# Optimization experiments

Hardware: AMD Instinct MI355X
Metric: run time of the kernel (lower is better)

The kernel has to match this reference:

```python
import jax, jax.numpy as jnp
import numpy as np

N, E, F, H, C, G = 50000, 600000, 128, 128, 10, 500
NUM_GIN = 3
BN_EPS = 1e-5


def _bn(x, gamma, beta):
    # BatchNorm1d in training mode: batch statistics over node/graph dim
    m = jnp.mean(x, axis=0)
    v = jnp.mean((x - m) ** 2, axis=0)
    return (x - m) * jax.lax.rsqrt(v + BN_EPS) * gamma + beta


def setup_inputs() -> dict:
    key = jax.random.key(0)
    ks = jax.random.split(key, 16)
    s = 1.0 / np.sqrt(H)
    inp = {
        "x": jax.random.normal(ks[0], (N, F), dtype=jnp.float32),
        "edge_index": jax.random.randint(ks[1], (2, E), 0, N),
        "batch": jnp.sort(jax.random.randint(ks[2], (N,), 0, G)),
        # bn_feat
        "gamma_feat": jnp.ones((F,), jnp.float32),
        "beta_feat": jnp.full((F,), 1e-4, jnp.float32),
        # conv_feat (GCNConv gfn=True -> pure linear)
        "W_feat": jax.random.uniform(ks[3], (F, H), jnp.float32, -s, s),
        "b_feat": jnp.zeros((H,), jnp.float32),
        # GIN conv MLPs, stacked over 3 layers
        "gin_W1": jax.random.uniform(ks[4], (NUM_GIN, H, H), jnp.float32, -s, s),
        "gin_b1": jnp.zeros((NUM_GIN, H), jnp.float32),
        "gin_gamma": jnp.ones((NUM_GIN, H), jnp.float32),
        "gin_beta": jnp.full((NUM_GIN, H), 1e-4, jnp.float32),
        "gin_W2": jax.random.uniform(ks[5], (NUM_GIN, H, H), jnp.float32, -s, s),
        "gin_b2": jnp.zeros((NUM_GIN, H), jnp.float32),
        # one FC block (num_fc_layers=2 -> 1 bn+lin)
        "gamma_fc": jnp.ones((H,), jnp.float32),
        "beta_fc": jnp.full((H,), 1e-4, jnp.float32),
        "W_fc": jax.random.uniform(ks[6], (H, H), jnp.float32, -s, s),
        "b_fc": jnp.zeros((H,), jnp.float32),
        # bn_hidden + classifier
        "gamma_h": jnp.ones((H,), jnp.float32),
        "beta_h": jnp.full((H,), 1e-4, jnp.float32),
        "W_cls": jax.random.uniform(ks[7], (H, C), jnp.float32, -s, s),
        "b_cls": jnp.zeros((C,), jnp.float32),
    }
    return inp


def reference(x, gamma_feat, beta_feat, W_feat, b_feat,
              gin_W1, gin_b1, gin_gamma, gin_beta, gin_W2, gin_b2,
              gamma_fc, beta_fc, W_fc, b_fc,
              gamma_h, beta_h, W_cls, b_cls,
              edge_index, batch):
    src, dst = edge_index[0], edge_index[1]
    h = _bn(x, gamma_feat, beta_feat)
    h = jax.nn.relu(h @ W_feat + b_feat)  # GCNConv gfn=True == Linear
    for i in range(NUM_GIN):
        # GIN aggregation: (1+eps)*x + sum_{j->i} x_j, eps=0
        agg = jnp.zeros_like(h).at[dst].add(h[src])
        z = h + agg
        z = jax.nn.relu(_bn(z @ gin_W1[i] + gin_b1[i], gin_gamma[i], gin_beta[i]))
        h = jax.nn.relu(z @ gin_W2[i] + gin_b2[i])
    g = jax.ops.segment_sum(h, batch, num_segments=G)  # global_add_pool -> [G,H]
    g = jax.nn.relu(_bn(g, gamma_fc, beta_fc) @ W_fc + b_fc)
    g = _bn(g, gamma_h, beta_h)
    logits = g @ W_cls + b_cls
    return jax.nn.log_softmax(logits, axis=-1)
```

## Files before the change

### kernel.cpp

```cpp
#include <hip/hip_runtime.h>
#include <math.h>

#define N_NODES 50000
#define N_EDGES 600000
#define HDIM 128
#define NCLS 10
#define NGRAPH 500
#define BN_EPS 1e-5f
#define SCAN_BLOCKS 196

typedef short bf16x8 __attribute__((ext_vector_type(8)));
typedef float f32x4 __attribute__((ext_vector_type(4)));

__global__ void colstats_kernel(const float* __restrict__ X, int M, float* __restrict__ stats) {
    int col = threadIdx.x & 127;
    int sub = threadIdx.x >> 7;
    float s = 0.f, sq = 0.f;
    for (int r = blockIdx.x * 2 + sub; r < M; r += gridDim.x * 2) {
        float v = X[(size_t)r * HDIM + col];
        s += v; sq += v * v;
    }
    atomicAdd(&stats[col], s);
    atomicAdd(&stats[HDIM + col], sq);
}

__global__ void hist_kernel(const int* __restrict__ ei, int* __restrict__ counts) {
    int e = blockIdx.x * 256 + threadIdx.x;
    if (e < N_EDGES) atomicAdd(&counts[ei[N_EDGES + e]], 1);
}

__global__ __launch_bounds__(256) void scan1_kernel(const int* __restrict__ counts,
                                                    int* __restrict__ partial,
                                                    int* __restrict__ blockSums) {
    __shared__ int tmp[256];
    int tid = threadIdx.x;
    int i = blockIdx.x * 256 + tid;
    int v = (i < N_NODES) ? counts[i] : 0;
    tmp[tid] = v;
    __syncthreads();
#pragma unroll
    for (int off = 1; off < 256; off <<= 1) {
        int t = (tid >= off) ? tmp[tid - off] : 0;
        __syncthreads();
        tmp[tid] += t;
        __syncthreads();
    }
    if (i < N_NODES) partial[i] = tmp[tid] - v;
    if (tid == 255) blockSums[blockIdx.x] = tmp[255];
}

__global__ __launch_bounds__(256) void scan2_kernel(const int* __restrict__ blockSums,
                                                    int* __restrict__ blockBase) {
    __shared__ int tmp[256];
    int tid = threadIdx.x;
    int v = (tid < SCAN_BLOCKS) ? blockSums[tid] : 0;
    tmp[tid] = v;
    __syncthreads();
#pragma unroll
    for (int off = 1; off < 256; off <<= 1) {
        int t = (tid >= off) ? tmp[tid - off] : 0;
        __syncthreads();
        tmp[tid] += t;
        __syncthreads();
    }
    if (tid < SCAN_BLOCKS) blockBase[tid] = tmp[tid] - v;
}

__global__ __launch_bounds__(256) void scan3_kernel(const int* __restrict__ partial,
                                                    const int* __restrict__ blockBase,
                                                    int* __restrict__ offsets,
                                                    int* __restrict__ cursor) {
    int i = blockIdx.x * 256 + threadIdx.x;
    if (i < N_NODES) {
        int o = partial[i] + blockBase[blockIdx.x];
        offsets[i] = o;
        cursor[i] = o;
    }
    if (i == 0) offsets[N_NODES] = N_EDGES;
}

__global__ void fill_kernel(const int* __restrict__ ei, int* __restrict__ cursor, int* __restrict__ csr) {
    int e = blockIdx.x * 256 + threadIdx.x;
    if (e < N_EDGES) {
        int d = ei[N_EDGES + e];
        int pos = atomicAdd(&cursor[d], 1);
        csr[pos] = ei[e];
    }
}

__global__ __launch_bounds__(256) void agg_kernel(const float* __restrict__ h,
                                                  const int* __restrict__ offsets,
                                                  const int* __restrict__ csr,
                                                  float* __restrict__ z) {
    int node = (blockIdx.x * 256 + threadIdx.x) >> 6;
    int lane = threadIdx.x & 63;
    if (node >= N_NODES) return;
    int c0 = lane * 2;
    int beg = offsets[node], end = offsets[node + 1];
    const float2 self = *(const float2*)&h[(size_t)node * HDIM + c0];
    float ax = self.x, ay = self.y;
    for (int j = beg; j < end; j += 64) {
        int cnt = min(64, end - j);
        int sl = (j + lane < end) ? csr[j + lane] : 0;
        int t = 0;
        for (; t + 4 <= cnt; t += 4) {
            int s0 = __shfl(sl, t, 64);
            int s1 = __shfl(sl, t + 1, 64);
            int s2 = __shfl(sl, t + 2, 64);
            int s3 = __shfl(sl, t + 3, 64);
            float2 v0 = *(const float2*)&h[(size_t)s0 * HDIM + c0];
            float2 v1 = *(const float2*)&h[(size_t)s1 * HDIM + c0];
            float2 v2 = *(const float2*)&h[(size_t)s2 * HDIM + c0];
            float2 v3 = *(const float2*)&h[(size_t)s3 * HDIM + c0];
            ax += v0.x + v1.x + v2.x + v3.x;
            ay += v0.y + v1.y + v2.y + v3.y;
        }
        for (; t < cnt; t++) {
            int s = __shfl(sl, t, 64);
            float2 hv = *(const float2*)&h[(size_t)s * HDIM + c0];
            ax += hv.x; ay += hv.y;
        }
    }
    float2 o; o.x = ax; o.y = ay;
    *(float2*)&z[(size_t)node * HDIM + c0] = o;
}

__global__ __launch_bounds__(128) void segsum2_kernel(const float* __restrict__ h,
                                                      const int* __restrict__ batch,
                                                      float* __restrict__ g) {
    int b = blockIdx.x;
    int tid = threadIdx.x;
    __shared__ int bounds[2];
    if (tid < 2) {
        int target = b + tid;
        int lo = 0, hi = N_NODES;
        while (lo < hi) {
            int mid = (lo + hi) >> 1;
            if (batch[mid] < target) lo = mid + 1; else hi = mid;
        }
        bounds[tid] = lo;
    }
    __syncthreads();
    int beg = bounds[0], end = bounds[1];
    float s = 0.f;
    for (int r = beg; r < end; r++) s += h[(size_t)r * HDIM + tid];
    g[b * HDIM + tid] = s;
}

__device__ inline void dekker_split(float v, unsigned short& hi, unsigned short& lo) {
    unsigned u = __float_as_uint(v);
    hi = (unsigned short)(u >> 16);
    float flo = v - __uint_as_float(u & 0xffff0000u);
    lo = (unsigned short)(__float_as_uint(flo) >> 16);
}

__global__ __launch_bounds__(256) void prep_w(const float* __restrict__ W1,
                                              const float* __restrict__ W2,
                                              unsigned short* __restrict__ wh,
                                              unsigned short* __restrict__ wl) {
    int m = blockIdx.x;
    const float* src = (m < 3) ? (W1 + m * HDIM * HDIM) : (W2 + (m - 3) * HDIM * HDIM);
    unsigned short* dh = wh + m * HDIM * HDIM;
    unsigned short* dl = wl + m * HDIM * HDIM;
    for (int i = threadIdx.x; i < HDIM * HDIM; i += 256) {
        int n = i >> 7, k = i & 127;
        float v = src[k * HDIM + n];
        unsigned short h16, l16;
        dekker_split(v, h16, l16);
        dh[i] = h16; dl[i] = l16;
    }
}

__global__ __launch_bounds__(256) void prep_feat(const float* __restrict__ W,
                                                 const float* __restrict__ bfeat,
                                                 const float* __restrict__ stats,
                                                 const float* __restrict__ gamma,
                                                 const float* __restrict__ beta,
                                                 float invCnt,
                                                 unsigned short* __restrict__ dh,
                                                 unsigned short* __restrict__ dl,
                                                 float* __restrict__ biasF) {
    __shared__ float aP[HDIM], bP[HDIM];
    int tid = threadIdx.x;
    if (tid < HDIM) {
        float m = stats[tid] * invCnt;
        float v = stats[HDIM + tid] * invCnt - m * m;
        float a = gamma[tid] * rsqrtf(v + BN_EPS);
        aP[tid] = a;
        bP[tid] = beta[tid] - m * a;
    }
    __syncthreads();
    for (int i = tid; i < HDIM * HDIM; i += 256) {
        int n = i >> 7, k = i & 127;
        float v = aP[k] * W[k * HDIM + n];
        unsigned short h16, l16;
        dekker_split(v, h16, l16);
        dh[i] = h16; dl[i] = l16;
    }
    if (tid < HDIM) {
        float acc = bfeat[tid];
        for (int k = 0; k < HDIM; k++) acc = fmaf(bP[k], W[k * HDIM + tid], acc);
        biasF[tid] = acc;
    }
}

template <int MODE>
__global__ __launch_bounds__(256, 2) void mfma_gemm(const float* __restrict__ A,
                                                    const unsigned short* __restrict__ Bh,
                                                    const unsigned short* __restrict__ Bl,
                                                    const float* __restrict__ bias,
                                                    float* __restrict__ C, int M,
                                                    const float* __restrict__ statsPre,
                                                    const float* __restrict__ gammaPre,
                                                    const float* __restrict__ betaPre,
                                                    float invCnt,
                                                    float* __restrict__ statsOut) {
    const int tid = threadIdx.x;
    const int w = tid >> 6, l = tid & 63;
    const int q = l >> 4, c16 = l & 15;
    const int rb = blockIdx.x * 128 + w * 32;

    int rowA[2];
#pragma unroll
    for (int rt = 0; rt < 2; rt++) rowA[rt] = min(rb + rt * 16 + c16, M - 1);

    float bs[8];
#pragma unroll
    for (int c = 0; c < 8; c++) bs[c] = bias[c * 16 + c16];

    f32x4 acc[2][8];
#pragma unroll
    for (int rt = 0; rt < 2; rt++)
#pragma unroll
        for (int c = 0; c < 8; c++) acc[rt][c] = (f32x4){0.f, 0.f, 0.f, 0.f};

#pragma unroll
    for (int s = 0; s < 4; s++) {
        const int k0 = s * 32 + q * 8;
        float aK[8], bK[8];
        if (MODE == 2) {
#pragma unroll
            for (int j = 0; j < 8; j++) {
                int k = k0 + j;
                float m = statsPre[k] * invCnt;
                float var = statsPre[HDIM + k] * invCnt - m * m;
                float a = gammaPre[k] * rsqrtf(var + BN_EPS);
                aK[j] = a;
                bK[j] = betaPre[k] - m * a;
            }
        }
        bf16x8 ah[2], al[2];
#pragma unroll
        for (int rt = 0; rt < 2; rt++) {
            const float* ap = A + (size_t)rowA[rt] * HDIM + k0;
            float4 v0 = *(const float4*)ap;
            float4 v1 = *(const float4*)(ap + 4);
            float vv[8] = {v0.x, v0.y, v0.z, v0.w, v1.x, v1.y, v1.z, v1.w};
#pragma unroll
            for (int j = 0; j < 8; j++) {
                float v = vv[j];
                if (MODE == 2) v = fmaxf(fmaf(v, aK[j], bK[j]), 0.f);
                unsigned u = __float_as_uint(v);
                ah[rt][j] = (short)(u >> 16);
                float flo = v - __uint_as_float(u & 0xffff0000u);
                al[rt][j] = (short)(__float_as_uint(flo) >> 16);
            }
        }
#pragma unroll
        for (int c = 0; c < 8; c++) {
            const size_t bo = (size_t)(c * 16 + c16) * HDIM + k0;
            bf16x8 bh = *(const bf16x8*)(Bh + bo);
            bf16x8 bl = *(const bf16x8*)(Bl + bo);
#pragma unroll
            for (int rt = 0; rt < 2; rt++) {
                acc[rt][c] = __builtin_amdgcn_mfma_f32_16x16x32_bf16(ah[rt], bh, acc[rt][c], 0, 0, 0);
                acc[rt][c] = __builtin_amdgcn_mfma_f32_16x16x32_bf16(al[rt], bh, acc[rt][c], 0, 0, 0);
                acc[rt][c] = __builtin_amdgcn_mfma_f32_16x16x32_bf16(ah[rt], bl, acc[rt][c], 0, 0, 0);
            }
        }
    }

    float ssum[8], ssq[8];
    if (MODE == 1) {
#pragma unroll
        for (int c = 0; c < 8; c++) { ssum[c] = 0.f; ssq[c] = 0.f; }
    }
#pragma unroll
    for (int rt = 0; rt < 2; rt++) {
#pragma unroll
        for (int reg = 0; reg < 4; reg++) {
            int row = rb + rt * 16 + q * 4 + reg;
            if (row < M) {
                float* cp = C + (size_t)row * HDIM + c16;
#pragma unroll
                for (int c = 0; c < 8; c++) {
                    float v = acc[rt][c][reg] + bs[c];
                    if (MODE != 1) v = fmaxf(v, 0.f);
                    cp[c * 16] = v;
                    if (MODE == 1) { ssum[c] += v; ssq[c] += v * v; }
                }
            }
        }
    }
    if (MODE == 1) {
#pragma unroll
        for (int c = 0; c < 8; c++) {
            float s2 = ssum[c] + __shfl_xor(ssum[c], 16, 64);
            float s4 = s2 + __shfl_xor(s2, 32, 64);
            float t2 = ssq[c] + __shfl_xor(ssq[c], 16, 64);
            float t4 = t2 + __shfl_xor(t2, 32, 64);
            if (q == 0) {
                atomicAdd(&statsOut[c * 16 + c16], s4);
                atomicAdd(&statsOut[HDIM + c * 16 + c16], t4);
            }
        }
    }
}

template <bool PRE_A, bool PRE_B, bool RELU, bool STATS>
__global__ __launch_bounds__(256, 3) void gemm_bn(const float* A, const float* __restrict__ B,
                                                  const float* __restrict__ bias, float* C, int M,
                                                  const float* __restrict__ statsPre,
                                                  const float* __restrict__ gammaPre,
                                                  const float* __restrict__ betaPre,
                                                  float invCnt, float* __restrict__ statsOut) {
    __shared__ float At[64][65];
    __shared__ float Bs[64][128];
    __shared__ float aPre[128], bPre[128];

    const int tid = threadIdx.x;
    const int tx = tid & 15, ty = tid >> 4;
    const int r0 = blockIdx.x * 64;

    if (PRE_A || PRE_B) {
        if (tid < 128) {
            float m = statsPre[tid] * invCnt;
            float v = statsPre[128 + tid] * invCnt - m * m;
            float a = gammaPre[tid] * rsqrtf(v + BN_EPS);
            aPre[tid] = a;
            bPre[tid] = betaPre[tid] - m * a;
        }
        __syncthreads();
    }

    float acc[4][8];
#pragma unroll
    for (int i = 0; i < 4; i++)
#pragma unroll
        for (int j = 0; j < 8; j++) acc[i][j] = 0.f;

    float biasEff[8];
#pragma unroll
    for (int j = 0; j < 8; j++) biasEff[j] = bias[8 * tx + j];
    if (PRE_B) {
        for (int k = 0; k < 128; k++) {
            float bb = bPre[k];
            const float* Brow = B + (size_t)k * HDIM + 8 * tx;
#pragma unroll
            for (int j = 0; j < 8; j++) biasEff[j] = fmaf(bb, Brow[j], biasEff[j]);
        }
    }

    for (int kc = 0; kc < 128; kc += 64) {
#pragma unroll
        for (int i = 0; i < 4; i++) {
            int f4 = tid + i * 256;
            int row = f4 >> 4;
            int kg = f4 & 15;
            int grow = r0 + row;
            float4 av;
            if (grow < M) av = *(const float4*)(A + (size_t)grow * HDIM + kc + kg * 4);
            else av = make_float4(0.f, 0.f, 0.f, 0.f);
            if (PRE_A) {
                int kb = kc + kg * 4;
                av.x = fmaxf(fmaf(av.x, aPre[kb + 0], bPre[kb + 0]), 0.f);
                av.y = fmaxf(fmaf(av.y, aPre[kb + 1], bPre[kb + 1]), 0.f);
                av.z = fmaxf(fmaf(av.z, aPre[kb + 2], bPre[kb + 2]), 0.f);
                av.w = fmaxf(fmaf(av.w, aPre[kb + 3], bPre[kb + 3]), 0.f);
            }
            At[kg * 4 + 0][row] = av.x;
            At[kg * 4 + 1][row] = av.y;
            At[kg * 4 + 2][row] = av.z;
            At[kg * 4 + 3][row] = av.w;
        }
#pragma unroll
        for (int i = 0; i < 8; i++) {
            int f4 = tid + i * 256;
            int krow = f4 >> 5;
            int cg = f4 & 31;
            float4 bv = *(const float4*)(B + (size_t)(kc + krow) * HDIM + cg * 4);
            if (PRE_B) {
                float s = aPre[kc + krow];
                bv.x *= s; bv.y *= s; bv.z *= s; bv.w *= s;
            }
            *(float4*)&Bs[krow][cg * 4] = bv;
        }
        __syncthreads();
#pragma unroll 8
        for (int k = 0; k < 64; k++) {
            float av[4];
            av[0] = At[k][ty];
            av[1] = At[k][ty + 16];
            av[2] = At[k][ty + 32];
            av[3] = At[k][ty + 48];
            const float4 b0 = *(const float4*)&Bs[k][8 * tx];
            const float4 b1 = *(const float4*)&Bs[k][8 * tx + 4];
            float bv[8] = {b0.x, b0.y, b0.z, b0.w, b1.x, b1.y, b1.z, b1.w};
#pragma unroll
            for (int i = 0; i < 4; i++)
#pragma unroll
                for (int j = 0; j < 8; j++) acc[i][j] = fmaf(av[i], bv[j], acc[i][j]);
        }
        __syncthreads();
    }

    float s[8], sq[8];
    if (STATS) {
#pragma unroll
        for (int j = 0; j < 8; j++) { s[j] = 0.f; sq[j] = 0.f; }
    }
#pragma unroll
    for (int i = 0; i < 4; i++) {
        int grow = r0 + ty + 16 * i;
        if (grow < M) {
            float v[8];
#pragma unroll
            for (int j = 0; j < 8; j++) {
                v[j] = acc[i][j] + biasEff[j];
                if (RELU) v[j] = fmaxf(v[j], 0.f);
                if (STATS) { s[j] += v[j]; sq[j] += v[j] * v[j]; }
            }
            float4 o0 = make_float4(v[0], v[1], v[2], v[3]);
            float4 o1 = make_float4(v[4], v[5], v[6], v[7]);
            *(float4*)(C + (size_t)grow * HDIM + 8 * tx) = o0;
            *(float4*)(C + (size_t)grow * HDIM + 8 * tx + 4) = o1;
        }
    }
    if (STATS) {
        float* red = &At[0][0];
#pragma unroll
        for (int j = 0; j < 8; j++) {
            red[ty * 128 + 8 * tx + j] = s[j];
            red[2048 + ty * 128 + 8 * tx + j] = sq[j];
        }
        __syncthreads();
        if (tid < 128) {
            float t = 0.f;
#pragma unroll
            for (int u = 0; u < 16; u++) t += red[u * 128 + tid];
            atomicAdd(&statsOut[tid], t);
        } else {
            int col = tid - 128;
            float t = 0.f;
#pragma unroll
            for (int u = 0; u < 16; u++) t += red[2048 + u * 128 + col];
            atomicAdd(&statsOut[128 + col], t);
        }
    }
}

__global__ __launch_bounds__(256) void head_kernel(const float* __restrict__ g2,
                                                   const float* __restrict__ stats,
                                                   const float* __restrict__ gamma,
                                                   const float* __restrict__ beta,
                                                   const float* __restrict__ Wc,
                                                   const float* __restrict__ bc,
                                                   float* __restrict__ out, float invCnt) {
    __shared__ float Wf[HDIM * NCLS];
    __shared__ float bf[NCLS];
    __shared__ float aP[HDIM], bP[HDIM];
    const int tid = threadIdx.x;
    if (tid < HDIM) {
        float m = stats[tid] * invCnt;
        float v = stats[HDIM + tid] * invCnt - m * m;
        float a = gamma[tid] * rsqrtf(v + BN_EPS);
        aP[tid] = a;
        bP[tid] = beta[tid] - m * a;
    }
    __syncthreads();
    for (int idx = tid; idx < HDIM * NCLS; idx += 256) {
        int k = idx / NCLS;
        Wf[idx] = aP[k] * Wc[idx];
    }
    if (tid < NCLS) {
        float sv = bc[tid];
        for (int k = 0; k < HDIM; k++) sv = fmaf(bP[k], Wc[k * NCLS + tid], sv);
        bf[tid] = sv;
    }
    __syncthreads();
    int row = blockIdx.x * 256 + tid;
    if (row >= NGRAPH) return;
    float l[NCLS];
#pragma unroll
    for (int c = 0; c < NCLS; c++) l[c] = bf[c];
    for (int k = 0; k < HDIM; k++) {
        float gv = g2[row * HDIM + k];
#pragma unroll
        for (int c = 0; c < NCLS; c++) l[c] = fmaf(gv, Wf[k * NCLS + c], l[c]);
    }
    float mx = l[0];
#pragma unroll
    for (int c = 1; c < NCLS; c++) mx = fmaxf(mx, l[c]);
    float se = 0.f;
#pragma unroll
    for (int c = 0; c < NCLS; c++) se += expf(l[c] - mx);
    float lse = mx + logf(se);
#pragma unroll
    for (int c = 0; c < NCLS; c++) out[row * NCLS + c] = l[c] - lse;
}

extern "C" void kernel_launch(void* const* d_in, const int* in_sizes, int n_in,
                              void* d_out, int out_size, void* d_ws, size_t ws_size,
                              hipStream_t stream) {
    const float* x          = (const float*)d_in[0];
    const int*   ei         = (const int*)d_in[1];
    const int*   batch      = (const int*)d_in[2];
    const float* gamma_feat = (const float*)d_in[3];
    const float* beta_feat  = (const float*)d_in[4];
    const float* W_feat     = (const float*)d_in[5];
    const float* b_feat     = (const float*)d_in[6];
    const float* gin_W1     = (const float*)d_in[7];
    const float* gin_b1     = (const float*)d_in[8];
    const float* gin_gamma  = (const float*)d_in[9];
    const float* gin_beta   = (const float*)d_in[10];
    const float* gin_W2     = (const float*)d_in[11];
    const float* gin_b2     = (const float*)d_in[12];
    const float* gamma_fc   = (const float*)d_in[13];
    const float* beta_fc    = (const float*)d_in[14];
    const float* W_fc       = (const float*)d_in[15];
    const float* b_fc       = (const float*)d_in[16];
    const float* gamma_h    = (const float*)d_in[17];
    const float* beta_h     = (const float*)d_in[18];
    const float* W_cls      = (const float*)d_in[19];
    const float* b_cls      = (const float*)d_in[20];
    float* out = (float*)d_out;

    float* ws = (float*)d_ws;
    size_t off = 0;
    float* h  = ws + off; off += (size_t)N_NODES * HDIM;
    float* zy = ws + off; off += (size_t)N_NODES * HDIM;
    float* g2 = ws + off; off += NGRAPH * HDIM;
    float* g  = ws + off; off += NGRAPH * HDIM;
    size_t zstart = off;
    float* stats = ws + off; off += 256 * 6;
    int* counts = (int*)(ws + off); off += N_NODES;
    size_t zbytes = (off - zstart) * sizeof(float);
    int* offsets   = (int*)(ws + off); off += N_NODES + 1;
    int* cursor    = (int*)(ws + off); off += N_NODES;
    int* csr       = (int*)(ws + off); off += N_EDGES;
    int* partial   = (int*)(ws + off); off += N_NODES;
    int* blockSums = (int*)(ws + off); off += 256;
    int* blockBase = (int*)(ws + off); off += 256;
    off = (off + 3) & ~(size_t)3;
    unsigned short* wt_hi = (unsigned short*)(ws + off); off += 7 * HDIM * HDIM / 2;
    unsigned short* wt_lo = (unsigned short*)(ws + off); off += 7 * HDIM * HDIM / 2;
    float* biasF = ws + off; off += HDIM;

    float* statsX  = stats;
    float* statsYa[3] = {stats + 256, stats + 512, stats + 768};
    float* statsG  = stats + 1024;
    float* statsG2 = stats + 1280;

    hipMemsetAsync(stats, 0, zbytes, stream);

    const float invN = 1.f / (float)N_NODES;
    const float invG = 1.f / (float)NGRAPH;
    const int eblocks = (N_EDGES + 255) / 256;
    const int nwaves  = (N_NODES * 64 + 255) / 256;
    const int mblocks = (N_NODES + 127) / 128;

    prep_w<<<6, 256, 0, stream>>>(gin_W1, gin_W2, wt_hi, wt_lo);
    colstats_kernel<<<256, 256, 0, stream>>>(x, N_NODES, statsX);
    hist_kernel<<<eblocks, 256, 0, stream>>>(ei, counts);
    scan1_kernel<<<SCAN_BLOCKS, 256, 0, stream>>>(counts, partial, blockSums);
    scan2_kernel<<<1, 256, 0, stream>>>(blockSums, blockBase);
    scan3_kernel<<<SCAN_BLOCKS, 256, 0, stream>>>(partial, blockBase, offsets, cursor);
    fill_kernel<<<eblocks, 256, 0, stream>>>(ei, cursor, csr);
    prep_feat<<<1, 256, 0, stream>>>(W_feat, b_feat, statsX, gamma_feat, beta_feat, invN,
                                     wt_hi + 6 * HDIM * HDIM, wt_lo + 6 * HDIM * HDIM, biasF);

    mfma_gemm<0><<<mblocks, 256, 0, stream>>>(
        x, wt_hi + 6 * HDIM * HDIM, wt_lo + 6 * HDIM * HDIM, biasF, h, N_NODES,
        nullptr, nullptr, nullptr, invN, nullptr);

    for (int i = 0; i < 3; i++) {
        agg_kernel<<<nwaves, 256, 0, stream>>>(h, offsets, csr, zy);
        mfma_gemm<1><<<mblocks, 256, 0, stream>>>(
            zy, wt_hi + i * HDIM * HDIM, wt_lo + i * HDIM * HDIM, gin_b1 + i * HDIM,
            zy, N_NODES, nullptr, nullptr, nullptr, invN, statsYa[i]);
        mfma_gemm<2><<<mblocks, 256, 0, stream>>>(
            zy, wt_hi + (3 + i) * HDIM * HDIM, wt_lo + (3 + i) * HDIM * HDIM, gin_b2 + i * HDIM,
            h, N_NODES, statsYa[i], gin_gamma + i * HDIM, gin_beta + i * HDIM, invN, nullptr);
    }

    segsum2_kernel<<<NGRAPH, 128, 0, stream>>>(h, batch, g);
    colstats_kernel<<<8, 256, 0, stream>>>(g, NGRAPH, statsG);
    gemm_bn<false, true, true, true><<<(NGRAPH + 63) / 64, 256, 0, stream>>>(
        g, W_fc, b_fc, g2, NGRAPH, statsG, gamma_fc, beta_fc, invG, statsG2);
    head_kernel<<<2, 256, 0, stream>>>(g2, statsG2, gamma_h, beta_h, W_cls, b_cls, out, invG);
}
```

Measured before the change: 709.3 us.

## Store GEMM weights fragment-major and software-pipeline B loads in MFMA GEMM

Weights are now pre-split into a fragment-major layout so each lane's B fragment load is fully contiguous and coalesced. The GEMM drops to 16 rows per wave (64 per block) with occupancy hint raised to 4, preloads all A rows up front and prefetches B fragments four steps ahead in a rolling buffer. BN scale/shift for MODE 2 is computed once per block into shared memory instead of per-lane per-k. The aim is to hide global-load latency and cut redundant BN math, at the cost of reloading B per 64-row block (less B reuse per wave).

```diff
diff --git a/kernel.cpp b/kernel.cpp
--- a/kernel.cpp
+++ b/kernel.cpp
@@ -154,6 +154,12 @@
     lo = (unsigned short)(__float_as_uint(flo) >> 16);
 }
 
+__device__ inline void fragmajor_decode(int i, int& k, int& n) {
+    int j = i & 7, l = (i >> 3) & 63, c = (i >> 9) & 7, s = (i >> 12) & 3;
+    n = c * 16 + (l & 15);
+    k = s * 32 + (l >> 4) * 8 + j;
+}
+
 __global__ __launch_bounds__(256) void prep_w(const float* __restrict__ W1,
                                               const float* __restrict__ W2,
                                               unsigned short* __restrict__ wh,
@@ -163,10 +169,10 @@
     unsigned short* dh = wh + m * HDIM * HDIM;
     unsigned short* dl = wl + m * HDIM * HDIM;
     for (int i = threadIdx.x; i < HDIM * HDIM; i += 256) {
-        int n = i >> 7, k = i & 127;
-        float v = src[k * HDIM + n];
+        int k, n;
+        fragmajor_decode(i, k, n);
         unsigned short h16, l16;
-        dekker_split(v, h16, l16);
+        dekker_split(src[k * HDIM + n], h16, l16);
         dh[i] = h16; dl[i] = l16;
     }
 }
@@ -191,10 +197,10 @@
     }
     __syncthreads();
     for (int i = tid; i < HDIM * HDIM; i += 256) {
-        int n = i >> 7, k = i & 127;
-        float v = aP[k] * W[k * HDIM + n];
+        int k, n;
+        fragmajor_decode(i, k, n);
         unsigned short h16, l16;
-        dekker_split(v, h16, l16);
+        dekker_split(aP[k] * W[k * HDIM + n], h16, l16);
         dh[i] = h16; dl[i] = l16;
     }
     if (tid < HDIM) {
@@ -205,7 +211,7 @@
 }
 
 template <int MODE>
-__global__ __launch_bounds__(256, 2) void mfma_gemm(const float* __restrict__ A,
+__global__ __launch_bounds__(256, 4) void mfma_gemm(const float* __restrict__ A,
                                                     const unsigned short* __restrict__ Bh,
                                                     const unsigned short* __restrict__ Bl,
                                                     const float* __restrict__ bias,
@@ -215,90 +221,103 @@
                                                     const float* __restrict__ betaPre,
                                                     float invCnt,
                                                     float* __restrict__ statsOut) {
+    __shared__ float sA[HDIM], sB[HDIM];
     const int tid = threadIdx.x;
     const int w = tid >> 6, l = tid & 63;
     const int q = l >> 4, c16 = l & 15;
-    const int rb = blockIdx.x * 128 + w * 32;
-
-    int rowA[2];
-#pragma unroll
-    for (int rt = 0; rt < 2; rt++) rowA[rt] = min(rb + rt * 16 + c16, M - 1);
-
-    float bs[8];
-#pragma unroll
-    for (int c = 0; c < 8; c++) bs[c] = bias[c * 16 + c16];
-
-    f32x4 acc[2][8];
-#pragma unroll
-    for (int rt = 0; rt < 2; rt++)
-#pragma unroll
-        for (int c = 0; c < 8; c++) acc[rt][c] = (f32x4){0.f, 0.f, 0.f, 0.f};
-
+    const int rb = blockIdx.x * 64 + w * 16;
+
+    if (MODE == 2) {
+        if (tid < HDIM) {
+            float m = statsPre[tid] * invCnt;
+            float var = statsPre[HDIM + tid] * invCnt - m * m;
+            float a = gammaPre[tid] * rsqrtf(var + BN_EPS);
+            sA[tid] = a;
+            sB[tid] = betaPre[tid] - m * a;
+        }
+        __syncthreads();
+    }
+
+    const int rowA = min(rb + c16, M - 1);
+    const float* ap = A + (size_t)rowA * HDIM + q * 8;
+    float4 araw[4][2];
 #pragma unroll
     for (int s = 0; s < 4; s++) {
-        const int k0 = s * 32 + q * 8;
-        float aK[8], bK[8];
-        if (MODE == 2) {
-#pragma unroll
-            for (int j = 0; j < 8; j++) {
-                int k = k0 + j;
-                float m = statsPre[k] * invCnt;
-                float var = statsPre[HDIM + k] * invCnt - m * m;
-                float a = gammaPre[k] * rsqrtf(var + BN_EPS);
-                aK[j] = a;
-                bK[j] = betaPre[k] - m * a;
+        araw[s][0] = *(const float4*)(ap + s * 32);
+        araw[s][1] = *(const float4*)(ap + s * 32 + 4);
+    }
+
+    const unsigned short* bhp = Bh + (size_t)l * 8;
+    const unsigned short* blp = Bl + (size_t)l * 8;
+    bf16x8 bhBuf[4], blBuf[4];
+#pragma unroll
+    for (int t = 0; t < 4; t++) {
+        bhBuf[t] = *(const bf16x8*)(bhp + (size_t)t * 512);
+        blBuf[t] = *(const bf16x8*)(blp + (size_t)t * 512);
+    }
+
+    f32x4 acc[8];
+#pragma unroll
+    for (int c = 0; c < 8; c++) acc[c] = (f32x4){0.f, 0.f, 0.f, 0.f};
+
+    bf16x8 ah, al;
+#pragma unroll
+    for (int t = 0; t < 32; t++) {
+        const int s = t >> 3, c = t & 7, b = t & 3;
+        if (c == 0) {
+            const int k0 = s * 32 + q * 8;
+            float vv[8] = {araw[s][0].x, araw[s][0].y, araw[s][0].z, araw[s][0].w,
+                           araw[s][1].x, araw[s][1].y, araw[s][1].z, araw[s][1].w};
+            float aK[8], bK[8];
+            if (MODE == 2) {
+                float4 a0 = *(const float4*)&sA[k0];
+                float4 a1 = *(const float4*)&sA[k0 + 4];
+                float4 b0 = *(const float4*)&sB[k0];
+                float4 b1 = *(const float4*)&sB[k0 + 4];
+                aK[0] = a0.x; aK[1] = a0.y; aK[2] = a0.z; aK[3] = a0.w;
+                aK[4] = a1.x; aK[5] = a1.y; aK[6] = a1.z; aK[7] = a1.w;
+                bK[0] = b0.x; bK[1] = b0.y; bK[2] = b0.z; bK[3] = b0.w;
+                bK[4] = b1.x; bK[5] = b1.y; bK[6] = b1.z; bK[7] = b1.w;
             }
-        }
-        bf16x8 ah[2], al[2];
-#pragma unroll
-        for (int rt = 0; rt < 2; rt++) {
-            const float* ap = A + (size_t)rowA[rt] * HDIM + k0;
-            float4 v0 = *(const float4*)ap;
-            float4 v1 = *(const float4*)(ap + 4);
-            float vv[8] = {v0.x, v0.y, v0.z, v0.w, v1.x, v1.y, v1.z, v1.w};
 #pragma unroll
             for (int j = 0; j < 8; j++) {
                 float v = vv[j];
                 if (MODE == 2) v = fmaxf(fmaf(v, aK[j], bK[j]), 0.f);
                 unsigned u = __float_as_uint(v);
-                ah[rt][j] = (short)(u >> 16);
+                ah[j] = (short)(u >> 16);
                 float flo = v - __uint_as_float(u & 0xffff0000u);
-                al[rt][j] = (short)(__float_as_uint(flo) >> 16);
+                al[j] = (short)(__float_as_uint(flo) >> 16);
             }
         }
-#pragma unroll
-        for (int c = 0; c < 8; c++) {
-            const size_t bo = (size_t)(c * 16 + c16) * HDIM + k0;
-            bf16x8 bh = *(const bf16x8*)(Bh + bo);
-            bf16x8 bl = *(const bf16x8*)(Bl + bo);
-#pragma unroll
-            for (int rt = 0; rt < 2; rt++) {
-                acc[rt][c] = __builtin_amdgcn_mfma_f32_16x16x32_bf16(ah[rt], bh, acc[rt][c], 0, 0, 0);
-                acc[rt][c] = __builtin_amdgcn_mfma_f32_16x16x32_bf16(al[rt], bh, acc[rt][c], 0, 0, 0);
-                acc[rt][c] = __builtin_amdgcn_mfma_f32_16x16x32_bf16(ah[rt], bl, acc[rt][c], 0, 0, 0);
-            }
-        }
-    }
-
+        f32x4 a0 = __builtin_amdgcn_mfma_f32_16x16x32_bf16(ah, bhBuf[b], acc[c], 0, 0, 0);
+        a0 = __builtin_amdgcn_mfma_f32_16x16x32_bf16(al, bhBuf[b], a0, 0, 0, 0);
+        a0 = __builtin_amdgcn_mfma_f32_16x16x32_bf16(ah, blBuf[b], a0, 0, 0, 0);
+        acc[c] = a0;
+        if (t < 28) {
+            bhBuf[b] = *(const bf16x8*)(bhp + (size_t)(t + 4) * 512);
+            blBuf[b] = *(const bf16x8*)(blp + (size_t)(t + 4) * 512);
+        }
+    }
+
+    float bsv[8];
+#pragma unroll
+    for (int c = 0; c < 8; c++) bsv[c] = bias[c * 16 + c16];
     float ssum[8], ssq[8];
     if (MODE == 1) {
 #pragma unroll
         for (int c = 0; c < 8; c++) { ssum[c] = 0.f; ssq[c] = 0.f; }
     }
 #pragma unroll
-    for (int rt = 0; rt < 2; rt++) {
-#pragma unroll
-        for (int reg = 0; reg < 4; reg++) {
-            int row = rb + rt * 16 + q * 4 + reg;
-            if (row < M) {
-                float* cp = C + (size_t)row * HDIM + c16;
-#pragma unroll
-                for (int c = 0; c < 8; c++) {
-                    float v = acc[rt][c][reg] + bs[c];
-                    if (MODE != 1) v = fmaxf(v, 0.f);
-                    cp[c * 16] = v;
-                    if (MODE == 1) { ssum[c] += v; ssq[c] += v * v; }
-                }
+    for (int reg = 0; reg < 4; reg++) {
+        int row = rb + q * 4 + reg;
+        if (row < M) {
+            float* cp = C + (size_t)row * HDIM + c16;
+#pragma unroll
+            for (int c = 0; c < 8; c++) {
+                float v = acc[c][reg] + bsv[c];
+                if (MODE != 1) v = fmaxf(v, 0.f);
+                cp[c * 16] = v;
+                if (MODE == 1) { ssum[c] += v; ssq[c] += v * v; }
             }
         }
     }
@@ -567,7 +586,7 @@
     const float invG = 1.f / (float)NGRAPH;
     const int eblocks = (N_EDGES + 255) / 256;
     const int nwaves  = (N_NODES * 64 + 255) / 256;
-    const int mblocks = (N_NODES + 127) / 128;
+    const int mblocks = (N_NODES + 63) / 64;
 
     prep_w<<<6, 256, 0, stream>>>(gin_W1, gin_W2, wt_hi, wt_lo);
     colstats_kernel<<<256, 256, 0, stream>>>(x, N_NODES, statsX);
```

After: 796.8 us. +12.3%, slower.
